# Kernel optimization log

Measured on AMD Instinct MI355X. Metric: run time of the kernel, lower is better.

## Reference

```python
import jax, jax.numpy as jnp
import numpy as np


def setup_inputs() -> dict:
    key = jax.random.key(0)
    ks = jax.random.split(key, 6)
    num_nodes, H, B = 500000, 128, 100000
    node_ids = jnp.arange(B, dtype=jnp.int64 if jax.config.jax_enable_x64 else jnp.int32)
    messages = jax.random.normal(ks[0], (B, H), dtype=jnp.float32)
    memory = jax.random.normal(ks[1], (num_nodes, H), dtype=jnp.float32)
    # PyTorch GRUCell params: weight_ih/weight_hh [3H, H], biases [3H]
    s = 1.0 / np.sqrt(H)
    W_ih = jax.random.uniform(ks[2], (3 * H, H), minval=-s, maxval=s, dtype=jnp.float32)
    W_hh = jax.random.uniform(ks[3], (3 * H, H), minval=-s, maxval=s, dtype=jnp.float32)
    b_ih = jax.random.uniform(ks[4], (3 * H,), minval=-s, maxval=s, dtype=jnp.float32)
    b_hh = jax.random.uniform(ks[5], (3 * H,), minval=-s, maxval=s, dtype=jnp.float32)
    return {"node_ids": node_ids, "messages": messages, "memory": memory,
            "W_ih": W_ih, "W_hh": W_hh, "b_ih": b_ih, "b_hh": b_hh}


def _gru_cell(x, h, W_ih, W_hh, b_ih, b_hh):
    # gi/gh: [B, 3H]; chunk order in torch GRUCell is (r, z, n)
    gi = x @ W_ih.T + b_ih
    gh = h @ W_hh.T + b_hh
    i_r, i_z, i_n = jnp.split(gi, 3, axis=-1)
    h_r, h_z, h_n = jnp.split(gh, 3, axis=-1)
    r = jax.nn.sigmoid(i_r + h_r)
    z = jax.nn.sigmoid(i_z + h_z)
    n = jnp.tanh(i_n + r * h_n)
    return (1.0 - z) * n + z * h


def reference(node_ids, messages, memory, W_ih, W_hh, b_ih, b_hh):
    # gather per-node memory, GRU update, scatter back (update_memory)
    current = memory[node_ids]                              # [B, H] gather
    updated = _gru_cell(messages, current, W_ih, W_hh, b_ih, b_hh)
    new_memory = memory.at[node_ids].set(updated)           # [N, H] scatter
    return new_memory
```

## Files before the change

kernel.cpp:

```cpp
#include <hip/hip_runtime.h>
#include <hip/hip_bf16.h>

typedef __bf16 bf16x8 __attribute__((ext_vector_type(8)));
typedef float  f32x4  __attribute__((ext_vector_type(4)));

#define GRU_H 128

__device__ inline bf16x8 load_frag_f32(const float* p) {
    float4 a = *reinterpret_cast<const float4*>(p);
    float4 b = *reinterpret_cast<const float4*>(p + 4);
    bf16x8 r;
    r[0] = (__bf16)a.x; r[1] = (__bf16)a.y; r[2] = (__bf16)a.z; r[3] = (__bf16)a.w;
    r[4] = (__bf16)b.x; r[5] = (__bf16)b.y; r[6] = (__bf16)b.z; r[7] = (__bf16)b.w;
    return r;
}

__device__ inline float sigmoidf_(float x) { return 1.f / (1.f + __expf(-x)); }
__device__ inline float tanhf_(float x)    { return 1.f - 2.f / (__expf(2.f * x) + 1.f); }

__global__ __launch_bounds__(512, 2) void gru_update_kernel(
    const int*   __restrict__ node_ids,
    const float* __restrict__ messages,
    const float* __restrict__ memory,
    const float* __restrict__ W_ih,
    const float* __restrict__ W_hh,
    const float* __restrict__ b_ih,
    const float* __restrict__ b_hh,
    float*       __restrict__ out,
    int B)
{
    const int wave = threadIdx.x >> 6;
    const int lane = threadIdx.x & 63;
    const int l15  = lane & 15;
    const int lg   = lane >> 4;
    const int col  = wave * 16 + l15;

    bf16x8 bfrag[6][4];
    #pragma unroll
    for (int g = 0; g < 3; ++g) {
        #pragma unroll
        for (int ks = 0; ks < 4; ++ks) {
            const int off = (g * GRU_H + col) * GRU_H + ks * 32 + lg * 8;
            bfrag[g][ks]     = load_frag_f32(W_ih + off);
            bfrag[g + 3][ks] = load_frag_f32(W_hh + off);
        }
    }
    const float bi_r = b_ih[col], bi_z = b_ih[GRU_H + col], bi_n = b_ih[2 * GRU_H + col];
    const float bh_r = b_hh[col], bh_z = b_hh[GRU_H + col], bh_n = b_hh[2 * GRU_H + col];

    const int nchunks = (B + 15) >> 4;
    for (int c = blockIdx.x; c < nchunks; c += gridDim.x) {
        const int rb = c * 16;
        int rowA = rb + l15;
        if (rowA >= B) rowA = B - 1;
        const int gidA = node_ids[rowA];

        bf16x8 ax[4], ah[4];
        #pragma unroll
        for (int ks = 0; ks < 4; ++ks) {
            ax[ks] = load_frag_f32(messages + (size_t)rowA * GRU_H + ks * 32 + lg * 8);
            ah[ks] = load_frag_f32(memory   + (size_t)gidA * GRU_H + ks * 32 + lg * 8);
        }

        f32x4 acc[6];
        #pragma unroll
        for (int g = 0; g < 6; ++g) acc[g] = (f32x4){0.f, 0.f, 0.f, 0.f};

        #pragma unroll
        for (int ks = 0; ks < 4; ++ks) {
            acc[0] = __builtin_amdgcn_mfma_f32_16x16x32_bf16(ax[ks], bfrag[0][ks], acc[0], 0, 0, 0);
            acc[1] = __builtin_amdgcn_mfma_f32_16x16x32_bf16(ax[ks], bfrag[1][ks], acc[1], 0, 0, 0);
            acc[2] = __builtin_amdgcn_mfma_f32_16x16x32_bf16(ax[ks], bfrag[2][ks], acc[2], 0, 0, 0);
            acc[3] = __builtin_amdgcn_mfma_f32_16x16x32_bf16(ah[ks], bfrag[3][ks], acc[3], 0, 0, 0);
            acc[4] = __builtin_amdgcn_mfma_f32_16x16x32_bf16(ah[ks], bfrag[4][ks], acc[4], 0, 0, 0);
            acc[5] = __builtin_amdgcn_mfma_f32_16x16x32_bf16(ah[ks], bfrag[5][ks], acc[5], 0, 0, 0);
        }

        #pragma unroll
        for (int r = 0; r < 4; ++r) {
            const int row = rb + lg * 4 + r;
            if (row < B) {
                const int gid = node_ids[row];
                const float h = memory[(size_t)gid * GRU_H + col];
                const float rg = sigmoidf_((acc[0][r] + bi_r) + (acc[3][r] + bh_r));
                const float zg = sigmoidf_((acc[1][r] + bi_z) + (acc[4][r] + bh_z));
                const float ng = tanhf_((acc[2][r] + bi_n) + rg * (acc[5][r] + bh_n));
                out[(size_t)gid * GRU_H + col] = (1.f - zg) * ng + zg * h;
            }
        }
    }
}

extern "C" void kernel_launch(void* const* d_in, const int* in_sizes, int n_in,
                              void* d_out, int out_size, void* d_ws, size_t ws_size,
                              hipStream_t stream) {
    const int*   node_ids = (const int*)d_in[0];
    const float* messages = (const float*)d_in[1];
    const float* memory   = (const float*)d_in[2];
    const float* W_ih     = (const float*)d_in[3];
    const float* W_hh     = (const float*)d_in[4];
    const float* b_ih     = (const float*)d_in[5];
    const float* b_hh     = (const float*)d_in[6];
    float* out = (float*)d_out;

    const int B = in_sizes[0];
    const int N = in_sizes[2] / GRU_H;

    hipMemcpyAsync(out, memory, (size_t)N * GRU_H * sizeof(float),
                   hipMemcpyDeviceToDevice, stream);

    const int nchunks = (B + 15) >> 4;
    int grid = nchunks < 512 ? nchunks : 512;
    gru_update_kernel<<<grid, 512, 0, stream>>>(node_ids, messages, memory,
                                                W_ih, W_hh, b_ih, b_hh, out, B);
}
```

Measured before the change: 588.7 us.

## Stage GRU input rows in LDS with coalesced loads and reverse-order memory copy

Replaces hipMemcpyAsync with a custom copy kernel that walks the memory array from the end toward the start. The likely intent is that the low-index rows the GRU kernel reads and writes next are the ones most recently touched and still in cache. The GRU kernel now loads 32-row tiles of messages and gathered memory into padded LDS with coalesced float4 loads, then builds MFMA fragments from LDS. The h value in the epilogue and the node ids are reused from LDS instead of being re-gathered from global memory. The grid grows to 1024 blocks, and each tile adds two __syncthreads and extra LDS usage that may cost occupancy.

```diff
diff --git a/kernel.cpp b/kernel.cpp
--- a/kernel.cpp
+++ b/kernel.cpp
@@ -5,8 +5,10 @@
 typedef float  f32x4  __attribute__((ext_vector_type(4)));
 
 #define GRU_H 128
+#define ROWS  32
+#define LDSP  132
 
-__device__ inline bf16x8 load_frag_f32(const float* p) {
+__device__ inline bf16x8 frag_from_lds(const float* p) {
     float4 a = *reinterpret_cast<const float4*>(p);
     float4 b = *reinterpret_cast<const float4*>(p + 4);
     bf16x8 r;
@@ -15,8 +17,19 @@
     return r;
 }
 
+__device__ inline bf16x8 frag_from_global(const float* p) { return frag_from_lds(p); }
+
 __device__ inline float sigmoidf_(float x) { return 1.f / (1.f + __expf(-x)); }
 __device__ inline float tanhf_(float x)    { return 1.f - 2.f / (__expf(2.f * x) + 1.f); }
+
+__global__ __launch_bounds__(256) void copy_rev_kernel(const float4* __restrict__ src,
+                                                       float4* __restrict__ dst, size_t n4) {
+    size_t stride = (size_t)gridDim.x * 256;
+    for (size_t i = (size_t)blockIdx.x * 256 + threadIdx.x; i < n4; i += stride) {
+        size_t j = n4 - 1 - i;
+        dst[j] = src[j];
+    }
+}
 
 __global__ __launch_bounds__(512, 2) void gru_update_kernel(
     const int*   __restrict__ node_ids,
@@ -29,6 +42,10 @@
     float*       __restrict__ out,
     int B)
 {
+    __shared__ float xs[ROWS][LDSP];
+    __shared__ float hs[ROWS][LDSP];
+    __shared__ int   ids[ROWS];
+
     const int wave = threadIdx.x >> 6;
     const int lane = threadIdx.x & 63;
     const int l15  = lane & 15;
@@ -37,57 +54,81 @@
 
     bf16x8 bfrag[6][4];
     #pragma unroll
-    for (int g = 0; g < 3; ++g) {
+    for (int g = 0; g < 3; ++g)
         #pragma unroll
         for (int ks = 0; ks < 4; ++ks) {
             const int off = (g * GRU_H + col) * GRU_H + ks * 32 + lg * 8;
-            bfrag[g][ks]     = load_frag_f32(W_ih + off);
-            bfrag[g + 3][ks] = load_frag_f32(W_hh + off);
+            bfrag[g][ks]     = frag_from_global(W_ih + off);
+            bfrag[g + 3][ks] = frag_from_global(W_hh + off);
         }
-    }
     const float bi_r = b_ih[col], bi_z = b_ih[GRU_H + col], bi_n = b_ih[2 * GRU_H + col];
     const float bh_r = b_hh[col], bh_z = b_hh[GRU_H + col], bh_n = b_hh[2 * GRU_H + col];
 
-    const int nchunks = (B + 15) >> 4;
+    const int nchunks = (B + ROWS - 1) / ROWS;
     for (int c = blockIdx.x; c < nchunks; c += gridDim.x) {
-        const int rb = c * 16;
-        int rowA = rb + l15;
-        if (rowA >= B) rowA = B - 1;
-        const int gidA = node_ids[rowA];
-
-        bf16x8 ax[4], ah[4];
-        #pragma unroll
-        for (int ks = 0; ks < 4; ++ks) {
-            ax[ks] = load_frag_f32(messages + (size_t)rowA * GRU_H + ks * 32 + lg * 8);
-            ah[ks] = load_frag_f32(memory   + (size_t)gidA * GRU_H + ks * 32 + lg * 8);
-        }
-
-        f32x4 acc[6];
-        #pragma unroll
-        for (int g = 0; g < 6; ++g) acc[g] = (f32x4){0.f, 0.f, 0.f, 0.f};
+        const int rb = c * ROWS;
 
         #pragma unroll
-        for (int ks = 0; ks < 4; ++ks) {
-            acc[0] = __builtin_amdgcn_mfma_f32_16x16x32_bf16(ax[ks], bfrag[0][ks], acc[0], 0, 0, 0);
-            acc[1] = __builtin_amdgcn_mfma_f32_16x16x32_bf16(ax[ks], bfrag[1][ks], acc[1], 0, 0, 0);
-            acc[2] = __builtin_amdgcn_mfma_f32_16x16x32_bf16(ax[ks], bfrag[2][ks], acc[2], 0, 0, 0);
-            acc[3] = __builtin_amdgcn_mfma_f32_16x16x32_bf16(ah[ks], bfrag[3][ks], acc[3], 0, 0, 0);
-            acc[4] = __builtin_amdgcn_mfma_f32_16x16x32_bf16(ah[ks], bfrag[4][ks], acc[4], 0, 0, 0);
-            acc[5] = __builtin_amdgcn_mfma_f32_16x16x32_bf16(ah[ks], bfrag[5][ks], acc[5], 0, 0, 0);
+        for (int s = 0; s < 2; ++s) {
+            const int f4  = threadIdx.x + s * 512;
+            const int row = f4 >> 5;
+            const int c4  = f4 & 31;
+            const int grow = rb + row;
+            if (grow < B) {
+                const int gid = node_ids[grow];
+                if (c4 == 0) ids[row] = gid;
+                *reinterpret_cast<float4*>(&xs[row][c4 * 4]) =
+                    *reinterpret_cast<const float4*>(&messages[(size_t)grow * GRU_H + c4 * 4]);
+                *reinterpret_cast<float4*>(&hs[row][c4 * 4]) =
+                    *reinterpret_cast<const float4*>(&memory[(size_t)gid * GRU_H + c4 * 4]);
+            } else {
+                float4 z = {0.f, 0.f, 0.f, 0.f};
+                *reinterpret_cast<float4*>(&xs[row][c4 * 4]) = z;
+                *reinterpret_cast<float4*>(&hs[row][c4 * 4]) = z;
+            }
         }
+        __syncthreads();
 
         #pragma unroll
-        for (int r = 0; r < 4; ++r) {
-            const int row = rb + lg * 4 + r;
-            if (row < B) {
-                const int gid = node_ids[row];
-                const float h = memory[(size_t)gid * GRU_H + col];
-                const float rg = sigmoidf_((acc[0][r] + bi_r) + (acc[3][r] + bh_r));
-                const float zg = sigmoidf_((acc[1][r] + bi_z) + (acc[4][r] + bh_z));
-                const float ng = tanhf_((acc[2][r] + bi_n) + rg * (acc[5][r] + bh_n));
-                out[(size_t)gid * GRU_H + col] = (1.f - zg) * ng + zg * h;
+        for (int sub = 0; sub < 2; ++sub) {
+            const int rbase = sub * 16;
+
+            bf16x8 ax[4], ah[4];
+            #pragma unroll
+            for (int ks = 0; ks < 4; ++ks) {
+                ax[ks] = frag_from_lds(&xs[rbase + l15][ks * 32 + lg * 8]);
+                ah[ks] = frag_from_lds(&hs[rbase + l15][ks * 32 + lg * 8]);
+            }
+
+            f32x4 acc[6];
+            #pragma unroll
+            for (int g = 0; g < 6; ++g) acc[g] = (f32x4){0.f, 0.f, 0.f, 0.f};
+
+            #pragma unroll
+            for (int ks = 0; ks < 4; ++ks) {
+                acc[0] = __builtin_amdgcn_mfma_f32_16x16x32_bf16(ax[ks], bfrag[0][ks], acc[0], 0, 0, 0);
+                acc[1] = __builtin_amdgcn_mfma_f32_16x16x32_bf16(ax[ks], bfrag[1][ks], acc[1], 0, 0, 0);
+                acc[2] = __builtin_amdgcn_mfma_f32_16x16x32_bf16(ax[ks], bfrag[2][ks], acc[2], 0, 0, 0);
+                acc[3] = __builtin_amdgcn_mfma_f32_16x16x32_bf16(ah[ks], bfrag[3][ks], acc[3], 0, 0, 0);
+                acc[4] = __builtin_amdgcn_mfma_f32_16x16x32_bf16(ah[ks], bfrag[4][ks], acc[4], 0, 0, 0);
+                acc[5] = __builtin_amdgcn_mfma_f32_16x16x32_bf16(ah[ks], bfrag[5][ks], acc[5], 0, 0, 0);
+            }
+
+            #pragma unroll
+            for (int r = 0; r < 4; ++r) {
+                const int row  = rbase + lg * 4 + r;
+                const int grow = rb + row;
+                if (grow < B) {
+                    const int gid = ids[row];
+                    const float h  = hs[row][col];
+                    const float rg = sigmoidf_((acc[0][r] + bi_r) + (acc[3][r] + bh_r));
+                    const float zg = sigmoidf_((acc[1][r] + bi_z) + (acc[4][r] + bh_z));
+                    const float ng = tanhf_((acc[2][r] + bi_n) + rg * (acc[5][r] + bh_n));
+                    out[(size_t)gid * GRU_H + col] = (1.f - zg) * ng + zg * h;
+                }
             }
         }
+        __syncthreads();
     }
 }
 
@@ -106,11 +147,11 @@
     const int B = in_sizes[0];
     const int N = in_sizes[2] / GRU_H;
 
-    hipMemcpyAsync(out, memory, (size_t)N * GRU_H * sizeof(float),
-                   hipMemcpyDeviceToDevice, stream);
+    const size_t n4 = (size_t)N * GRU_H / 4;
+    copy_rev_kernel<<<2048, 256, 0, stream>>>((const float4*)memory, (float4*)out, n4);
 
-    const int nchunks = (B + 15) >> 4;
-    int grid = nchunks < 512 ? nchunks : 512;
+    const int nchunks = (B + ROWS - 1) / ROWS;
+    int grid = nchunks < 1024 ? nchunks : 1024;
     gru_update_kernel<<<grid, 512, 0, stream>>>(node_ids, messages, memory,
                                                 W_ih, W_hh, b_ih, b_hh, out, B);
 }
```

New measurement: 596.5 us. No clear change (+1.3%).
